# Optimization experiments

Hardware: AMD Instinct MI355X
Metric: run time of the kernel (lower is better)

Reference implementation:

```python
import jax, jax.numpy as jnp
import numpy as np

B, H, S, D, HID, A = 16384, 15, 32, 256, 256, 6


def setup_inputs() -> dict:
    key = jax.random.key(0)
    ks = iter(jax.random.split(key, 32))
    rn = lambda shape, scale=1.0: jax.random.normal(next(ks), shape, dtype=jnp.float32) * scale
    w = 0.05  # small weight init scale
    return {
        "stoch_state": rn((B, S)),
        "gru_state": rn((B, D)),
        "act_noise": rn((H, B, A)),
        "stoch_noise": rn((H, B, S)),
        "W_a0": rn((HID, S + D), w), "b_a0": jnp.zeros((HID,), jnp.float32),
        "W_a1": rn((HID, HID), w),   "b_a1": jnp.zeros((HID,), jnp.float32),
        "W_am": rn((A, HID), w),     "b_am": jnp.zeros((A,), jnp.float32),
        "W_as": rn((A, HID), w),     "b_as": jnp.zeros((A,), jnp.float32),
        "W_img": rn((HID, S + A), w), "b_img": jnp.zeros((HID,), jnp.float32),
        "W_ih": rn((3 * D, HID), w), "b_ih": jnp.zeros((3 * D,), jnp.float32),
        "W_hh": rn((3 * D, D), w),   "b_hh": jnp.zeros((3 * D,), jnp.float32),
        "W_p0": rn((HID, D), w),     "b_p0": jnp.zeros((HID,), jnp.float32),
        "W_pm": rn((S, HID), w),     "b_pm": jnp.zeros((S,), jnp.float32),
        "W_ps": rn((S, HID), w),     "b_ps": jnp.zeros((S,), jnp.float32),
    }


def _lin(x, W, b):
    return x @ W.T + b


def _gru_cell(x, h, W_ih, b_ih, W_hh, b_hh):
    # torch.nn.GRUCell gate layout: [reset, update, new]
    gi = _lin(x, W_ih, b_ih)
    gh = _lin(h, W_hh, b_hh)
    ir, iz, inn = jnp.split(gi, 3, axis=-1)
    hr, hz, hn = jnp.split(gh, 3, axis=-1)
    r = jax.nn.sigmoid(ir + hr)
    z = jax.nn.sigmoid(iz + hz)
    n = jnp.tanh(inn + r * hn)
    return (1.0 - z) * n + z * h


def dream(stoch_state, gru_state, act_noise, stoch_noise,
          W_a0, b_a0, W_a1, b_a1, W_am, b_am, W_as, b_as,
          W_img, b_img, W_ih, b_ih, W_hh, b_hh,
          W_p0, b_p0, W_pm, b_pm, W_ps, b_ps):
    def step(carry, noise):
        stoch, gru = carry
        an, sn = noise
        state = jnp.concatenate([stoch, gru], axis=-1)
        # action model on detached state (as in original dream())
        sd = jax.lax.stop_gradient(state)
        ah = jax.nn.elu(_lin(sd, W_a0, b_a0))
        ah = jax.nn.elu(_lin(ah, W_a1, b_a1))
        a_mean = _lin(ah, W_am, b_am)
        a_std = jax.nn.softplus(_lin(ah, W_as, b_as))
        action = a_mean + a_std * an  # rsample
        # img1 MLP
        x = jax.nn.elu(_lin(jnp.concatenate([stoch, action], axis=-1), W_img, b_img))
        # GRU cell
        gru = _gru_cell(x, gru, W_ih, b_ih, W_hh, b_hh)
        # prior model rsample
        ph = jax.nn.elu(_lin(gru, W_p0, b_p0))
        p_mean = _lin(ph, W_pm, b_pm)
        p_std = jax.nn.softplus(_lin(ph, W_ps, b_ps))
        stoch = p_mean + p_std * sn
        out = jnp.concatenate([stoch, gru], axis=-1)  # [B, S+D]
        return (stoch, gru), out

    _, states = jax.lax.scan(step, (stoch_state, gru_state), (act_noise, stoch_noise))
    return states  # [H, B, S+D]


def reference(stoch_state, gru_state, act_noise, stoch_noise,
              W_a0, b_a0, W_a1, b_a1, W_am, b_am, W_as, b_as,
              W_img, b_img, W_ih, b_ih, W_hh, b_hh,
              W_p0, b_p0, W_pm, b_pm, W_ps, b_ps):
    return dream(stoch_state, gru_state, act_noise, stoch_noise,
                 W_a0, b_a0, W_a1, b_a1, W_am, b_am, W_as, b_as,
                 W_img, b_img, W_ih, b_ih, W_hh, b_hh,
                 W_p0, b_p0, W_pm, b_pm, W_ps, b_ps)
```

## Files before the change

### kernel.cpp

```cpp
#include <hip/hip_runtime.h>
#include <hip/hip_bf16.h>

#define MFMA_BF16 __builtin_amdgcn_mfma_f32_16x16x32_bf16

typedef __attribute__((ext_vector_type(8))) short short8;
typedef __attribute__((ext_vector_type(4))) float f32x4;

#define NB 16384
#define NH 15
#define NS 32
#define ND 256
#define NHID 256
#define NA 6

#define OFF_A0   0
#define OFF_A1   73728
#define OFF_AMS  139264
#define OFF_IMG  143360
#define OFF_IH   159744
#define OFF_HH   356352
#define OFF_P0   552960
#define OFF_PMS  618496
#define W_TOTAL  634880

__device__ __forceinline__ short f2b(float v){ __hip_bfloat16 b = __float2bfloat16(v); return __builtin_bit_cast(short, b); }
__device__ __forceinline__ float b2f(short s){ return __bfloat162float(__builtin_bit_cast(__hip_bfloat16, s)); }
__device__ __forceinline__ float sigm(float x){ return 1.f/(1.f + __expf(-x)); }
__device__ __forceinline__ float softp(float x){ return fmaxf(x,0.f) + log1pf(__expf(-fabsf(x))); }
__device__ __forceinline__ float eluf(float x){ return x>0.f ? x : (__expf(x)-1.f); }

__device__ __forceinline__ void decode_frag(int m, int KB, int& row, int& k){
  int tidx = m >> 9, w = m & 511;
  int lane = w >> 3, e = w & 7;
  int t = tidx / KB, kb = tidx - t*KB;
  row = t*16 + (lane & 15);
  k   = kb*32 + ((lane >> 4) << 3) + e;
}

__global__ void pack_w(const float* __restrict__ a0, const float* __restrict__ a1,
                       const float* __restrict__ am, const float* __restrict__ as,
                       const float* __restrict__ img, const float* __restrict__ ih,
                       const float* __restrict__ hh, const float* __restrict__ p0,
                       const float* __restrict__ pm, const float* __restrict__ ps,
                       short* __restrict__ ws){
  int i = blockIdx.x*256 + threadIdx.x;
  if (i >= W_TOTAL) return;
  int row, k; float v;
  if (i < OFF_A1){        decode_frag(i - OFF_A0, 9, row, k);  v = a0[row*288 + k]; }
  else if (i < OFF_AMS){  decode_frag(i - OFF_A1, 8, row, k);  v = a1[row*256 + k]; }
  else if (i < OFF_IMG){  decode_frag(i - OFF_AMS, 8, row, k);
                          v = row<6 ? am[row*256+k] : (row<12 ? as[(row-6)*256+k] : 0.f); }
  else if (i < OFF_IH){   decode_frag(i - OFF_IMG, 2, row, k);
                          v = k<38 ? img[row*38 + k] : 0.f; }
  else if (i < OFF_HH){   decode_frag(i - OFF_IH, 8, row, k);  v = ih[row*256 + k]; }
  else if (i < OFF_P0){   decode_frag(i - OFF_HH, 8, row, k);  v = hh[row*256 + k]; }
  else if (i < OFF_PMS){  decode_frag(i - OFF_P0, 8, row, k);  v = p0[row*256 + k]; }
  else {                  decode_frag(i - OFF_PMS, 8, row, k);
                          v = row<32 ? pm[row*256+k] : ps[(row-32)*256+k]; }
  ws[i] = f2b(v);
}

template<int KB, bool ELU>
__device__ __forceinline__ void dense_slice(const short* __restrict__ Ab, int astr,
                                            const short* __restrict__ W,
                                            const float* __restrict__ bias,
                                            short* __restrict__ Ob,
                                            int tbase, int n0, int lane, int lk){
  f32x4 acc[2][2] = {};
  const short* ap = Ab + (lane & 15)*astr + lk*8;
  const int astep = 16*astr;
  const short* wl = W + lane*8;
  #pragma unroll
  for (int kb=0; kb<KB; ++kb){
    short8 a0 = *(const short8*)(ap + kb*32);
    short8 a1 = *(const short8*)(ap + astep + kb*32);
    #pragma unroll
    for (int j=0; j<2; ++j){
      short8 b = *(const short8*)(wl + ((tbase + j)*KB + kb)*512);
      acc[0][j] = MFMA_BF16(a0, b, acc[0][j], 0, 0, 0);
      acc[1][j] = MFMA_BF16(a1, b, acc[1][j], 0, 0, 0);
    }
  }
  #pragma unroll
  for (int mt=0; mt<2; ++mt){
    #pragma unroll
    for (int j=0; j<2; ++j){
      int n = n0 + j*16;
      float bs = bias[n];
      #pragma unroll
      for (int i=0; i<4; ++i){
        int row = mt*16 + lk*4 + i;
        float v = acc[mt][j][i] + bs;
        Ob[row*264 + n] = f2b(ELU ? eluf(v) : v);
      }
    }
  }
}

__global__ __launch_bounds__(256, 2) void dream_kernel(
    const float* __restrict__ stoch0, const float* __restrict__ gru0,
    const float* __restrict__ anoise, const float* __restrict__ snoise,
    const short* __restrict__ ws,
    const float* __restrict__ b_a0, const float* __restrict__ b_a1,
    const float* __restrict__ b_am, const float* __restrict__ b_as,
    const float* __restrict__ b_img, const float* __restrict__ b_ih,
    const float* __restrict__ b_hh, const float* __restrict__ b_p0,
    const float* __restrict__ b_pm, const float* __restrict__ b_ps,
    float* __restrict__ out)
{
  __shared__ short bufA[32*264];
  __shared__ short bufB[32*264];
  __shared__ short bufC[32*264];
  __shared__ short simg[32*72];

  const int tid   = threadIdx.x;
  const int wid   = tid >> 6;
  const int lane  = tid & 63;
  const int lrow  = lane & 15;
  const int lk    = lane >> 4;
  const int r0    = blockIdx.x * 32;
  const int tb0   = wid * 4;
  const int n00   = wid * 64 + lrow;
  const int tb1   = wid * 4 + 2;
  const int n01   = wid * 64 + 32 + lrow;

  for (int idx = tid; idx < 32*256; idx += 256){
    int r = idx >> 8, c = idx & 255;
    bufA[r*264 + c] = f2b(gru0[(size_t)(r0+r)*256 + c]);
  }
  for (int idx = tid; idx < 32*32; idx += 256){
    int r = idx >> 5, c = idx & 31;
    simg[r*72 + c]      = f2b(stoch0[(size_t)(r0+r)*32 + c]);
    simg[r*72 + 32 + c] = 0;
  }
  __syncthreads();

  short* G = bufA;
  short* X = bufB;
  short* Y = bufC;

  for (int h = 0; h < NH; ++h){
    #pragma unroll 1
    for (int half=0; half<2; ++half){
      const int tbase = half ? tb1 : tb0;
      const int n0    = half ? n01 : n00;
      f32x4 acc[2][2] = {};
      const short* ai = simg + lrow*72  + lk*8;
      const short* ag = G    + lrow*264 + lk*8;
      const short* wl = ws + OFF_A0 + lane*8;
      #pragma unroll
      for (int kb=0; kb<9; ++kb){
        short8 a0 = (kb==0) ? *(const short8*)ai : *(const short8*)(ag + (kb-1)*32);
        short8 a1 = (kb==0) ? *(const short8*)(ai + 16*72) : *(const short8*)(ag + 16*264 + (kb-1)*32);
        #pragma unroll
        for (int j=0; j<2; ++j){
          short8 b = *(const short8*)(wl + ((tbase + j)*9 + kb)*512);
          acc[0][j] = MFMA_BF16(a0, b, acc[0][j], 0, 0, 0);
          acc[1][j] = MFMA_BF16(a1, b, acc[1][j], 0, 0, 0);
        }
      }
      #pragma unroll
      for (int mt=0; mt<2; ++mt)
        #pragma unroll
        for (int j=0; j<2; ++j){
          int n = n0 + j*16;
          float bs = b_a0[n];
          #pragma unroll
          for (int i=0; i<4; ++i){
            int row = mt*16 + lk*4 + i;
            X[row*264 + n] = f2b(eluf(acc[mt][j][i] + bs));
          }
        }
    }
    __syncthreads();

    dense_slice<8,true>(X, 264, ws + OFF_A1, b_a1, Y, tb0, n00, lane, lk);
    dense_slice<8,true>(X, 264, ws + OFF_A1, b_a1, Y, tb1, n01, lane, lk);
    __syncthreads();

    f32x4 iacc[2][2][2];
    {
      const short* wlI = ws + OFF_IMG + lane*8;
      const short* ai  = simg + lrow*72 + lk*8;
      #pragma unroll
      for (int half=0; half<2; ++half){
        const int tbs = half ? tb1 : tb0;
        #pragma unroll
        for (int mt=0; mt<2; ++mt){
          short8 a = *(const short8*)(ai + mt*16*72);
          #pragma unroll
          for (int j=0; j<2; ++j){
            short8 b = *(const short8*)(wlI + ((tbs + j)*2 + 0)*512);
            f32x4 z = {};
            iacc[half][mt][j] = MFMA_BF16(a, b, z, 0, 0, 0);
          }
        }
      }
      if (wid < 2){
        const int mt = wid;
        f32x4 acc = {};
        const short* ap = Y + (mt*16+lrow)*264 + lk*8;
        const short* wl = ws + OFF_AMS + lane*8;
        #pragma unroll
        for (int kb=0; kb<8; ++kb){
          short8 a = *(const short8*)(ap + kb*32);
          short8 b = *(const short8*)(wl + kb*512);
          acc = MFMA_BF16(a, b, acc, 0, 0, 0);
        }
        float bs = (lrow<6) ? b_am[lrow] : (lrow<12 ? b_as[lrow-6] : 0.f);
        #pragma unroll
        for (int i=0; i<4; ++i){
          float raw = acc[i] + bs;
          float sp  = softp(raw);
          float spn = __shfl(sp, (lane & 48) | ((lrow + 6) & 15));
          if (lrow < 6){
            int row = mt*16 + lk*4 + i;
            size_t grow = r0 + row;
            float an = __builtin_nontemporal_load(&anoise[((size_t)h*NB + grow)*NA + lrow]);
            simg[row*72 + 32 + lrow] = f2b(raw + spn * an);
          }
        }
      }
    }
    __syncthreads();

    {
      const short* wlI = ws + OFF_IMG + lane*8;
      const short* ai  = simg + lrow*72 + 32 + lk*8;
      #pragma unroll
      for (int half=0; half<2; ++half){
        const int tbs = half ? tb1 : tb0;
        #pragma unroll
        for (int mt=0; mt<2; ++mt){
          short8 a = *(const short8*)(ai + mt*16*72);
          #pragma unroll
          for (int j=0; j<2; ++j){
            short8 b = *(const short8*)(wlI + ((tbs + j)*2 + 1)*512);
            iacc[half][mt][j] = MFMA_BF16(a, b, iacc[half][mt][j], 0, 0, 0);
          }
        }
      }
      #pragma unroll
      for (int half=0; half<2; ++half){
        const int nb = half ? n01 : n00;
        #pragma unroll
        for (int mt=0; mt<2; ++mt)
          #pragma unroll
          for (int j=0; j<2; ++j){
            int n = nb + j*16;
            float bs = b_img[n];
            #pragma unroll
            for (int i=0; i<4; ++i){
              int row = mt*16 + lk*4 + i;
              X[row*264 + n] = f2b(eluf(iacc[half][mt][j][i] + bs));
            }
          }
      }
    }
    __syncthreads();

    {
      const short* wl_ih = ws + OFF_IH + lane*8;
      const short* wl_hh = ws + OFF_HH + lane*8;
      #pragma unroll 1
      for (int mtl=0; mtl<2; ++mtl){
        const int rbase = mtl*16;
        const short* xp = X + (rbase+lrow)*264 + lk*8;
        const short* gp = G + (rbase+lrow)*264 + lk*8;
        #pragma unroll 1
        for (int jj=0; jj<4; ++jj){
          f32x4 aR = {}, aZ = {}, aI = {}, aH = {};
          const int tr = wid*4 + jj;
          #pragma unroll
          for (int kb=0; kb<8; ++kb){
            short8 br = *(const short8*)(wl_ih + ((tr     )*8 + kb)*512);
            short8 bz = *(const short8*)(wl_ih + ((tr + 16)*8 + kb)*512);
            short8 bn = *(const short8*)(wl_ih + ((tr + 32)*8 + kb)*512);
            short8 cr = *(const short8*)(wl_hh + ((tr     )*8 + kb)*512);
            short8 cz = *(const short8*)(wl_hh + ((tr + 16)*8 + kb)*512);
            short8 ch = *(const short8*)(wl_hh + ((tr + 32)*8 + kb)*512);
            short8 ax = *(const short8*)(xp + kb*32);
            short8 ag = *(const short8*)(gp + kb*32);
            aR = MFMA_BF16(ax, br, aR, 0, 0, 0);
            aZ = MFMA_BF16(ax, bz, aZ, 0, 0, 0);
            aI = MFMA_BF16(ax, bn, aI, 0, 0, 0);
            aR = MFMA_BF16(ag, cr, aR, 0, 0, 0);
            aZ = MFMA_BF16(ag, cz, aZ, 0, 0, 0);
            aH = MFMA_BF16(ag, ch, aH, 0, 0, 0);
          }
          int c = wid*64 + jj*16 + lrow;
          float bir = b_ih[c]       + b_hh[c];
          float biz = b_ih[256 + c] + b_hh[256 + c];
          float bin = b_ih[512 + c];
          float bhn = b_hh[512 + c];
          #pragma unroll
          for (int i=0; i<4; ++i){
            int row = rbase + lk*4 + i;
            float hold = b2f(G[row*264 + c]);
            float r = sigm(aR[i] + bir);
            float z = sigm(aZ[i] + biz);
            float n = tanhf(aI[i] + bin + r*(aH[i] + bhn));
            float hnew = (1.f - z)*n + z*hold;
            Y[row*264 + c] = f2b(hnew);
            __builtin_nontemporal_store(hnew, &out[((size_t)h*NB + (size_t)(r0+row))*288 + 32 + c]);
          }
        }
      }
    }
    __syncthreads();

    dense_slice<8,true>(Y, 264, ws + OFF_P0, b_p0, X, tb0, n00, lane, lk);
    dense_slice<8,true>(Y, 264, ws + OFF_P0, b_p0, X, tb1, n01, lane, lk);
    __syncthreads();

    {
      const int mt = wid & 1;
      const int jp = wid >> 1;
      f32x4 accM = {}, accS = {};
      const short* ap = X + (mt*16+lrow)*264 + lk*8;
      const short* wl = ws + OFF_PMS + lane*8;
      #pragma unroll
      for (int kb=0; kb<8; ++kb){
        short8 a  = *(const short8*)(ap + kb*32);
        short8 bm = *(const short8*)(wl + ((jp    )*8 + kb)*512);
        short8 bs = *(const short8*)(wl + ((jp + 2)*8 + kb)*512);
        accM = MFMA_BF16(a, bm, accM, 0, 0, 0);
        accS = MFMA_BF16(a, bs, accS, 0, 0, 0);
      }
      int sc = jp*16 + lrow;
      float bm = b_pm[sc], bp = b_ps[sc];
      #pragma unroll
      for (int i=0; i<4; ++i){
        int row = mt*16 + lk*4 + i;
        size_t grow = r0 + row;
        float m  = accM[i] + bm;
        float sp = softp(accS[i] + bp);
        float sn = __builtin_nontemporal_load(&snoise[((size_t)h*NB + grow)*NS + sc]);
        float st = m + sp*sn;
        simg[row*72 + sc] = f2b(st);
        __builtin_nontemporal_store(st, &out[((size_t)h*NB + grow)*288 + sc]);
      }
    }
    __syncthreads();

    short* t = G; G = Y; Y = X; X = t;
  }
}

extern "C" void kernel_launch(void* const* d_in, const int* in_sizes, int n_in,
                              void* d_out, int out_size, void* d_ws, size_t ws_size,
                              hipStream_t stream){
  const float* stoch0 = (const float*)d_in[0];
  const float* gru0   = (const float*)d_in[1];
  const float* anoise = (const float*)d_in[2];
  const float* snoise = (const float*)d_in[3];
  const float* Wa0 = (const float*)d_in[4];   const float* ba0 = (const float*)d_in[5];
  const float* Wa1 = (const float*)d_in[6];   const float* ba1 = (const float*)d_in[7];
  const float* Wam = (const float*)d_in[8];   const float* bam = (const float*)d_in[9];
  const float* Was = (const float*)d_in[10];  const float* bas = (const float*)d_in[11];
  const float* Wimg= (const float*)d_in[12];  const float* bimg= (const float*)d_in[13];
  const float* Wih = (const float*)d_in[14];  const float* bih = (const float*)d_in[15];
  const float* Whh = (const float*)d_in[16];  const float* bhh = (const float*)d_in[17];
  const float* Wp0 = (const float*)d_in[18];  const float* bp0 = (const float*)d_in[19];
  const float* Wpm = (const float*)d_in[20];  const float* bpm = (const float*)d_in[21];
  const float* Wps = (const float*)d_in[22];  const float* bps = (const float*)d_in[23];
  short* ws  = (short*)d_ws;
  float* out = (float*)d_out;

  pack_w<<<(W_TOTAL + 255)/256, 256, 0, stream>>>(Wa0, Wa1, Wam, Was, Wimg, Wih, Whh, Wp0, Wpm, Wps, ws);
  dream_kernel<<<NB/32, 256, 0, stream>>>(stoch0, gru0, anoise, snoise, ws,
                                          ba0, ba1, bam, bas, bimg, bih, bhh, bp0, bpm, bps, out);
}
```

Measured before the change: 1.085 ms.

## Precompute gru part of action layer-0 early to overlap with prior head

Splits the first action-layer GEMM into a stoch part (k-block 0) and a gru part (k-blocks 1-8). The gru contribution for the next step is computed right after the new GRU state is written, inside the prior-head phase, and kept in registers. Only the small stoch part plus the ELU remain at the top of each step. This is meant to cut the serial dependency chain and shorten the critical path per step, at the cost of 32 more live accumulator registers, which may lower occupancy or cause spills.

```diff
diff --git a/kernel.cpp b/kernel.cpp
--- a/kernel.cpp
+++ b/kernel.cpp
@@ -139,38 +139,57 @@
   short* X = bufB;
   short* Y = bufC;
 
+  f32x4 a0acc[2][2][2];
+
+  {
+    const short* ag = G + lrow*264 + lk*8;
+    const short* wl = ws + OFF_A0 + lane*8;
+    #pragma unroll
+    for (int half=0; half<2; ++half){
+      const int tbs = half ? tb1 : tb0;
+      #pragma unroll
+      for (int mt=0; mt<2; ++mt)
+        #pragma unroll
+        for (int j=0; j<2; ++j)
+          a0acc[half][mt][j] = f32x4{0.f,0.f,0.f,0.f};
+      #pragma unroll
+      for (int kb=1; kb<9; ++kb){
+        short8 av0 = *(const short8*)(ag + (kb-1)*32);
+        short8 av1 = *(const short8*)(ag + 16*264 + (kb-1)*32);
+        #pragma unroll
+        for (int j=0; j<2; ++j){
+          short8 b = *(const short8*)(wl + ((tbs + j)*9 + kb)*512);
+          a0acc[half][0][j] = MFMA_BF16(av0, b, a0acc[half][0][j], 0, 0, 0);
+          a0acc[half][1][j] = MFMA_BF16(av1, b, a0acc[half][1][j], 0, 0, 0);
+        }
+      }
+    }
+  }
+
   for (int h = 0; h < NH; ++h){
-    #pragma unroll 1
-    for (int half=0; half<2; ++half){
-      const int tbase = half ? tb1 : tb0;
-      const int n0    = half ? n01 : n00;
-      f32x4 acc[2][2] = {};
-      const short* ai = simg + lrow*72  + lk*8;
-      const short* ag = G    + lrow*264 + lk*8;
+    {
+      const short* ai = simg + lrow*72 + lk*8;
       const short* wl = ws + OFF_A0 + lane*8;
-      #pragma unroll
-      for (int kb=0; kb<9; ++kb){
-        short8 a0 = (kb==0) ? *(const short8*)ai : *(const short8*)(ag + (kb-1)*32);
-        short8 a1 = (kb==0) ? *(const short8*)(ai + 16*72) : *(const short8*)(ag + 16*264 + (kb-1)*32);
+      short8 av0 = *(const short8*)ai;
+      short8 av1 = *(const short8*)(ai + 16*72);
+      #pragma unroll
+      for (int half=0; half<2; ++half){
+        const int tbs = half ? tb1 : tb0;
+        const int nb  = half ? n01 : n00;
         #pragma unroll
         for (int j=0; j<2; ++j){
-          short8 b = *(const short8*)(wl + ((tbase + j)*9 + kb)*512);
-          acc[0][j] = MFMA_BF16(a0, b, acc[0][j], 0, 0, 0);
-          acc[1][j] = MFMA_BF16(a1, b, acc[1][j], 0, 0, 0);
-        }
-      }
-      #pragma unroll
-      for (int mt=0; mt<2; ++mt)
-        #pragma unroll
-        for (int j=0; j<2; ++j){
-          int n = n0 + j*16;
+          short8 b = *(const short8*)(wl + ((tbs + j)*9 + 0)*512);
+          f32x4 acc0 = MFMA_BF16(av0, b, a0acc[half][0][j], 0, 0, 0);
+          f32x4 acc1 = MFMA_BF16(av1, b, a0acc[half][1][j], 0, 0, 0);
+          int n = nb + j*16;
           float bs = b_a0[n];
           #pragma unroll
           for (int i=0; i<4; ++i){
-            int row = mt*16 + lk*4 + i;
-            X[row*264 + n] = f2b(eluf(acc[mt][j][i] + bs));
-          }
-        }
+            X[(lk*4 + i)*264 + n]      = f2b(eluf(acc0[i] + bs));
+            X[(16 + lk*4 + i)*264 + n] = f2b(eluf(acc1[i] + bs));
+          }
+        }
+      }
     }
     __syncthreads();
 
@@ -314,6 +333,28 @@
     __syncthreads();
 
     {
+      const short* ag = Y + lrow*264 + lk*8;
+      const short* wlA = ws + OFF_A0 + lane*8;
+      #pragma unroll
+      for (int half=0; half<2; ++half){
+        const int tbs = half ? tb1 : tb0;
+        #pragma unroll
+        for (int mt=0; mt<2; ++mt)
+          #pragma unroll
+          for (int j=0; j<2; ++j)
+            a0acc[half][mt][j] = f32x4{0.f,0.f,0.f,0.f};
+        #pragma unroll
+        for (int kb=1; kb<9; ++kb){
+          short8 av0 = *(const short8*)(ag + (kb-1)*32);
+          short8 av1 = *(const short8*)(ag + 16*264 + (kb-1)*32);
+          #pragma unroll
+          for (int j=0; j<2; ++j){
+            short8 b = *(const short8*)(wlA + ((tbs + j)*9 + kb)*512);
+            a0acc[half][0][j] = MFMA_BF16(av0, b, a0acc[half][0][j], 0, 0, 0);
+            a0acc[half][1][j] = MFMA_BF16(av1, b, a0acc[half][1][j], 0, 0, 0);
+          }
+        }
+      }
       const int mt = wid & 1;
       const int jp = wid >> 1;
       f32x4 accM = {}, accS = {};
```

Result: slower. 1.252 ms (+15.4%).
